# Optimization experiments

Measured on AMD Instinct MI355X. Metric: run time of the kernel, lower is better.

Reference implementation:

```python
import jax, jax.numpy as jnp
import numpy as np

B, N, D = 8, 4096, 256
H = W = 64          # grid_size = img_size // patch_size = 256 // 4
WS = 8              # swin window size
NH = 8              # swin heads
M = 16              # fno modes
E = 4               # num experts
TD = 768            # text dim
HID = 1024          # mlp hidden = 4 * D
TK = 2              # top_k


def gelu(x):
    return jax.nn.gelu(x, approximate=False)


def layernorm(x, g, b, eps=1e-5):
    mu = x.mean(-1, keepdims=True)
    var = ((x - mu) ** 2).mean(-1, keepdims=True)
    return (x - mu) * jax.lax.rsqrt(var + eps) * g + b


def fno_expert(x, w1r, w1i, w2r, w2i, conv_w, conv_b):
    # x: [B, N, D] -> grid [B, D, H, W]
    xg = x.transpose(0, 2, 1).reshape(B, D, H, W)
    xft = jnp.fft.rfft2(xg)                      # [B, D, H, W//2+1] complex64
    w1 = w1r + 1j * w1i
    w2 = w2r + 1j * w2i
    top = jnp.einsum('bixy,ioxy->boxy', xft[:, :, :M, :M], w1)
    bot = jnp.einsum('bixy,ioxy->boxy', xft[:, :, -M:, :M], w2)
    out_ft = jnp.zeros((B, D, H, W // 2 + 1), dtype=xft.dtype)
    out_ft = out_ft.at[:, :, :M, :M].set(top).at[:, :, -M:, :M].set(bot)
    x1 = jnp.fft.irfft2(out_ft, s=(H, W))        # [B, D, H, W]
    x2 = jnp.einsum('bdhw,do->bohw', xg, conv_w) + conv_b[None, :, None, None]
    out = gelu(x1 + x2)
    return out.reshape(B, D, N).transpose(0, 2, 1) + x


def mlp_expert(x, w1, b1, w2, b2):
    return gelu(x @ w1 + b1) @ w2 + b2 + x


def window_attn_expert(x, ln1_g, ln1_b, qkv_w, qkv_b, out_w, out_b,
                       ln2_g, ln2_b, mw1, mb1, mw2, mb2):
    shortcut = x
    h = layernorm(x, ln1_g, ln1_b)
    # window partition: [B,H,W,C] -> [B*nW, WS*WS, C]
    h = h.reshape(B, H // WS, WS, W // WS, WS, D)
    h = h.transpose(0, 1, 3, 2, 4, 5).reshape(-1, WS * WS, D)
    # multi-head self attention (torch nn.MultiheadAttention semantics)
    qkv = h @ qkv_w + qkv_b                      # [Bw, L, 3D]
    q, k, v = jnp.split(qkv, 3, axis=-1)
    dh = D // NH
    def heads(t):
        return t.reshape(-1, WS * WS, NH, dh).transpose(0, 2, 1, 3)
    q, k, v = heads(q), heads(k), heads(v)
    scores = jnp.einsum('whld,whmd->whlm', q, k) / jnp.sqrt(jnp.float32(dh))
    attn = jax.nn.softmax(scores, axis=-1)
    o = jnp.einsum('whlm,whmd->whld', attn, v)
    o = o.transpose(0, 2, 1, 3).reshape(-1, WS * WS, D)
    o = o @ out_w + out_b
    # window reverse
    o = o.reshape(B, H // WS, W // WS, WS, WS, D)
    o = o.transpose(0, 1, 3, 2, 4, 5).reshape(B, N, D)
    x = o + shortcut
    h2 = layernorm(x, ln2_g, ln2_b)
    return x + (gelu(h2 @ mw1 + mb1) @ mw2 + mb2)


def setup_inputs() -> dict:
    key = jax.random.key(0)
    ks = jax.random.split(key, 24)
    rn = lambda k, s: jax.random.normal(k, s, jnp.float32) * 0.02
    fscale = 1.0 / (D * D)
    ru = lambda k: jax.random.uniform(k, (D, D, M, M), jnp.float32) * fscale
    return {
        'x': jax.random.normal(ks[0], (B, N, D), jnp.float32),
        'text_embedding': jax.random.normal(ks[1], (B, TD), jnp.float32),
        'gate_w1': rn(ks[2], (D + TD, D)), 'gate_b1': jnp.zeros((D,), jnp.float32),
        'gate_w2': rn(ks[3], (D, E)), 'gate_b2': jnp.zeros((E,), jnp.float32),
        'fno_w1r': ru(ks[4]), 'fno_w1i': ru(ks[5]),
        'fno_w2r': ru(ks[6]), 'fno_w2i': ru(ks[7]),
        'fno_conv_w': rn(ks[8], (D, D)), 'fno_conv_b': jnp.zeros((D,), jnp.float32),
        'mlp1_w1': rn(ks[9], (D, HID)), 'mlp1_b1': jnp.zeros((HID,), jnp.float32),
        'mlp1_w2': rn(ks[10], (HID, D)), 'mlp1_b2': jnp.zeros((D,), jnp.float32),
        'mlp2_w1': rn(ks[11], (D, HID)), 'mlp2_b1': jnp.zeros((HID,), jnp.float32),
        'mlp2_w2': rn(ks[12], (HID, D)), 'mlp2_b2': jnp.zeros((D,), jnp.float32),
        'wa_ln1_g': jnp.ones((D,), jnp.float32), 'wa_ln1_b': jnp.zeros((D,), jnp.float32),
        'wa_qkv_w': rn(ks[13], (D, 3 * D)), 'wa_qkv_b': jnp.zeros((3 * D,), jnp.float32),
        'wa_out_w': rn(ks[14], (D, D)), 'wa_out_b': jnp.zeros((D,), jnp.float32),
        'wa_ln2_g': jnp.ones((D,), jnp.float32), 'wa_ln2_b': jnp.zeros((D,), jnp.float32),
        'wa_mlp_w1': rn(ks[15], (D, HID)), 'wa_mlp_b1': jnp.zeros((HID,), jnp.float32),
        'wa_mlp_w2': rn(ks[16], (HID, D)), 'wa_mlp_b2': jnp.zeros((D,), jnp.float32),
    }


def reference(x, text_embedding, gate_w1, gate_b1, gate_w2, gate_b2,
              fno_w1r, fno_w1i, fno_w2r, fno_w2i, fno_conv_w, fno_conv_b,
              mlp1_w1, mlp1_b1, mlp1_w2, mlp1_b2,
              mlp2_w1, mlp2_b1, mlp2_w2, mlp2_b2,
              wa_ln1_g, wa_ln1_b, wa_qkv_w, wa_qkv_b, wa_out_w, wa_out_b,
              wa_ln2_g, wa_ln2_b, wa_mlp_w1, wa_mlp_b1, wa_mlp_w2, wa_mlp_b2):
    # --- gating ---
    feat = jnp.concatenate([x.mean(axis=1), text_embedding], axis=1)  # [B, D+TD]
    logits = jax.nn.relu(feat @ gate_w1 + gate_b1) @ gate_w2 + gate_b2  # [B, E]
    top_v, top_i = jax.lax.top_k(logits, TK)
    weights = jax.nn.softmax(top_v, axis=-1)                           # [B, TK]
    # per-expert combined weight: cw[b,e] = sum_k w[b,k] * (idx[b,k]==e)
    cw = (jax.nn.one_hot(top_i, E, dtype=x.dtype) * weights[..., None]).sum(axis=1)  # [B, E]
    # --- experts (FNO, MLP, WindowAttn, MLP) ---
    e0 = fno_expert(x, fno_w1r, fno_w1i, fno_w2r, fno_w2i, fno_conv_w, fno_conv_b)
    e1 = mlp_expert(x, mlp1_w1, mlp1_b1, mlp1_w2, mlp1_b2)
    e2 = window_attn_expert(x, wa_ln1_g, wa_ln1_b, wa_qkv_w, wa_qkv_b,
                            wa_out_w, wa_out_b, wa_ln2_g, wa_ln2_b,
                            wa_mlp_w1, wa_mlp_b1, wa_mlp_w2, wa_mlp_b2)
    e3 = mlp_expert(x, mlp2_w1, mlp2_b1, mlp2_w2, mlp2_b2)
    outs = jnp.stack([e0, e1, e2, e3])                                 # [E, B, N, D]
    final = jnp.einsum('be,ebnd->bnd', cw, outs)
    return final, weights
```

## Files before the change

### kernel.cpp

```cpp
#include <hip/hip_runtime.h>
#include <math.h>


#define NB 8
#define NN 4096
#define DD 256

typedef __attribute__((ext_vector_type(8))) short bf16x8;
typedef __attribute__((ext_vector_type(4))) float f32x4;

__device__ __forceinline__ float gelu_f(float v) {
    return 0.5f * v * (1.0f + erff(v * 0.7071067811865475f));
}
__device__ __forceinline__ ushort f2bf(float f) {
    uint32_t u = __float_as_uint(f);
    uint32_t r = (u + 0x7fffu + ((u >> 16) & 1u)) >> 16;
    return (ushort)r;
}
__device__ __forceinline__ float b2f(ushort h) {
    return __uint_as_float(((uint32_t)h) << 16);
}

__global__ void k_cvt_gate(const float* __restrict__ src, ushort* __restrict__ dst,
                           float* __restrict__ gp) {
    __shared__ float4 st[4][64];
    int blk = blockIdx.x;
    int t = threadIdx.x;
    int i = blk * 256 + t;
    float4 v = ((const float4*)src)[i];
    ushort4 o;
    o.x = f2bf(v.x); o.y = f2bf(v.y); o.z = f2bf(v.z); o.w = f2bf(v.w);
    ((ushort4*)dst)[i] = o;
    st[t >> 6][t & 63] = v;
    __syncthreads();
    if (t < 64) {
        float4 a = st[0][t], b = st[1][t], c = st[2][t], d = st[3][t];
        float4 s;
        s.x = a.x + b.x + c.x + d.x;
        s.y = a.y + b.y + c.y + d.y;
        s.z = a.z + b.z + c.z + d.z;
        s.w = a.w + b.w + c.w + d.w;
        ((float4*)(gp + (size_t)blk * 256))[t] = s;
    }
}

__global__ void __launch_bounds__(256) k_gate_mm(const float* __restrict__ gp,
        const float* __restrict__ text, const float* __restrict__ w1,
        const float* __restrict__ b1, float* __restrict__ h1) {
    __shared__ float fs[1024];
    int b = blockIdx.x, t = threadIdx.x;
    const float* base = gp + (size_t)b * 1024 * 256;
    float s0 = 0.f, s1 = 0.f, s2 = 0.f, s3 = 0.f;
    for (int j = 0; j < 1024; j += 4) {
        s0 += base[(j + 0) * 256 + t];
        s1 += base[(j + 1) * 256 + t];
        s2 += base[(j + 2) * 256 + t];
        s3 += base[(j + 3) * 256 + t];
    }
    fs[t] = (s0 + s1 + s2 + s3) * (1.0f / NN);
    for (int j = t; j < 768; j += 256) fs[256 + j] = text[b * 768 + j];
    __syncthreads();
    float acc = b1[t];
    for (int k = 0; k < 1024; ++k) acc += fs[k] * w1[k * 256 + t];
    h1[b * 256 + t] = fmaxf(acc, 0.f);
}

__global__ void k_gate_top(const float* __restrict__ h1, const float* __restrict__ w2,
                           const float* __restrict__ b2, float* __restrict__ cw,
                           float* __restrict__ wout) {
    __shared__ float lg[8][4];
    int t = threadIdx.x;
    if (t < 32) {
        int b = t >> 2, e = t & 3;
        float acc = b2[e];
        const float* h = h1 + b * 256;
        for (int k = 0; k < 256; ++k) acc += h[k] * w2[k * 4 + e];
        lg[b][e] = acc;
    }
    __syncthreads();
    if (t < 8) {
        int b = t;
        float v[4];
        #pragma unroll
        for (int e = 0; e < 4; ++e) v[e] = lg[b][e];
        int i0 = 0;
        #pragma unroll
        for (int e = 1; e < 4; ++e) if (v[e] > v[i0]) i0 = e;
        int i1 = -1;
        #pragma unroll
        for (int e = 0; e < 4; ++e) {
            if (e == i0) continue;
            if (i1 < 0 || v[e] > v[i1]) i1 = e;
        }
        float v0 = v[i0], v1 = v[i1];
        float e1v = expf(v1 - v0);
        float inv = 1.0f / (1.0f + e1v);
        float w0 = inv, w1v = e1v * inv;
        wout[b * 2 + 0] = w0;
        wout[b * 2 + 1] = w1v;
        float c[4] = {0.f, 0.f, 0.f, 0.f};
        c[i0] += w0; c[i1] += w1v;
        #pragma unroll
        for (int e = 0; e < 4; ++e) cw[b * 4 + e] = c[e];
    }
}

__global__ void k_wt_all(const float* s0, const float* s1, const float* s2,
        const float* s3, const float* s4, const float* s5, const float* s6,
        const float* s7, const float* s8,
        ushort* d0, ushort* d1, ushort* d2, ushort* d3, ushort* d4,
        ushort* d5, ushort* d6, ushort* d7, ushort* d8) {
    const float* srcs[9] = {s0, s1, s2, s3, s4, s5, s6, s7, s8};
    ushort* dsts[9] = {d0, d1, d2, d3, d4, d5, d6, d7, d8};
    const int Ks[9] = {256, 1024, 256, 1024, 256, 1024, 256, 256, 256};
    const int Ns[9] = {1024, 256, 1024, 256, 1024, 256, 768, 256, 256};
    __shared__ float tile[32][33];
    int j = blockIdx.z;
    int K = Ks[j], N = Ns[j];
    int tn = N >> 5, tk = K >> 5;
    int tid = blockIdx.x;
    if (tid >= tn * tk) return;
    int n0 = (tid % tn) * 32, k0 = (tid / tn) * 32;
    const float* src = srcs[j];
    ushort* dst = dsts[j];
    int tx = threadIdx.x, ty = threadIdx.y;
    #pragma unroll
    for (int i = 0; i < 4; ++i)
        tile[ty + i * 8][tx] = src[(size_t)(k0 + ty + i * 8) * N + n0 + tx];
    __syncthreads();
    #pragma unroll
    for (int i = 0; i < 4; ++i)
        dst[(size_t)(n0 + ty + i * 8) * K + k0 + tx] = f2bf(tile[tx][ty + i * 8]);
}

template<int MODE>
__global__ void __launch_bounds__(256) k_gemm(const ushort* __restrict__ A,
        const ushort* __restrict__ Bt, const float* __restrict__ bias,
        const float* __restrict__ res, float* __restrict__ outf,
        ushort* __restrict__ outb, const float* __restrict__ cw, int eidx,
        int K, int Ncols, size_t bsA, size_t bsB, size_t bsC) {
    __shared__ alignas(16) char smem[32768];
    ushort* sA = (ushort*)smem;
    ushort* sB = (ushort*)(smem + 16384);
    int z = blockIdx.z;
    A += z * bsA; Bt += z * bsB;
    if (outf) outf += z * bsC;
    if (outb) outb += z * bsC;
    int m0 = blockIdx.x * 128;
    int n0 = blockIdx.y * 128;
    int t = threadIdx.x;
    int lane = t & 63, wid = t >> 6;
    int wr = wid >> 1, wc = wid & 1;
    int rlo = lane & 15, khi = (lane >> 4) * 8;

    auto stage = [&](int buf, int k0) {
        const ushort* Ab = A + (size_t)m0 * K + k0;
        const ushort* Bb = Bt + (size_t)n0 * K + k0;
        #pragma unroll
        for (int h = 0; h < 2; ++h) {
            int s = t + h * 256;
            int row = s >> 2, kc = (s & 3) * 8;
            __builtin_amdgcn_global_load_lds(
                (const __attribute__((address_space(1))) void*)(Ab + (size_t)row * K + kc),
                (__attribute__((address_space(3))) void*)(sA + buf * 4096 + s * 8),
                16, 0, 0);
            __builtin_amdgcn_global_load_lds(
                (const __attribute__((address_space(1))) void*)(Bb + (size_t)row * K + kc),
                (__attribute__((address_space(3))) void*)(sB + buf * 4096 + s * 8),
                16, 0, 0);
        }
    };

    f32x4 acc[4][4];
    #pragma unroll
    for (int i = 0; i < 4; ++i)
        #pragma unroll
        for (int j = 0; j < 4; ++j) acc[i][j] = (f32x4){0.f, 0.f, 0.f, 0.f};

    int KT = K >> 5;
    stage(0, 0);
    int cur = 0;
    for (int kt = 0; kt < KT; ++kt) {
        __syncthreads();
        if (kt + 1 < KT) stage(cur ^ 1, (kt + 1) << 5);
        const ushort* Ap = sA + cur * 4096;
        const ushort* Bp = sB + cur * 4096;
        bf16x8 af[4], bfr[4];
        #pragma unroll
        for (int i = 0; i < 4; ++i) {
            af[i]  = *(const bf16x8*)(Ap + (wr * 64 + i * 16 + rlo) * 32 + khi);
            bfr[i] = *(const bf16x8*)(Bp + (wc * 64 + i * 16 + rlo) * 32 + khi);
        }
        #pragma unroll
        for (int i = 0; i < 4; ++i)
            #pragma unroll
            for (int j = 0; j < 4; ++j)
                acc[i][j] = __builtin_amdgcn_mfma_f32_16x16x32_bf16(af[i], bfr[j], acc[i][j], 0, 0, 0);
        cur ^= 1;
    }

    float bj4[4];
    if constexpr (MODE != 4 && MODE != 5) {
        #pragma unroll
        for (int nt = 0; nt < 4; ++nt) bj4[nt] = bias[n0 + wc * 64 + nt * 16 + rlo];
    }

    if constexpr (MODE == 0 || MODE == 1 || MODE == 5) {
        ushort* eb = (ushort*)smem;
        #pragma unroll
        for (int mt = 0; mt < 4; ++mt) {
            __syncthreads();
            #pragma unroll
            for (int nt = 0; nt < 4; ++nt) {
                int col = wc * 64 + nt * 16 + rlo;
                #pragma unroll
                for (int j = 0; j < 4; ++j) {
                    float v = acc[mt][nt][j];
                    if constexpr (MODE == 5)
                        v += bias[m0 + wr * 64 + mt * 16 + (lane >> 4) * 4 + j];
                    else
                        v += bj4[nt];
                    if (MODE == 0) v = gelu_f(v);
                    eb[(wr * 16 + (lane >> 4) * 4 + j) * 136 + col] = f2bf(v);
                }
            }
            __syncthreads();
            #pragma unroll
            for (int h = 0; h < 2; ++h) {
                int s = t + h * 256;
                int r = s >> 4, c = (s & 15) * 8;
                int grow = m0 + (r >> 4) * 64 + mt * 16 + (r & 15);
                *(uint4*)(outb + (size_t)grow * Ncols + n0 + c) = *(uint4*)&eb[r * 136 + c];
            }
        }
    } else {
        float* ep = (float*)smem;
        #pragma unroll
        for (int mt = 0; mt < 4; ++mt) {
            __syncthreads();
            #pragma unroll
            for (int nt = 0; nt < 4; ++nt) {
                int col = wc * 64 + nt * 16 + rlo;
                #pragma unroll
                for (int j = 0; j < 4; ++j) {
                    float v = acc[mt][nt][j];
                    if constexpr (MODE == 4)
                        v += bias[m0 + wr * 64 + mt * 16 + (lane >> 4) * 4 + j];
                    else
                        v += bj4[nt];
                    ep[(wr * 16 + (lane >> 4) * 4 + j) * 132 + col] = v;
                }
            }
            __syncthreads();
            #pragma unroll
            for (int h = 0; h < 4; ++h) {
                int s = t + h * 256;
                int r = s >> 5, c4 = (s & 31) * 4;
                int grow = m0 + (r >> 4) * 64 + mt * 16 + (r & 15);
                size_t g = (size_t)grow * Ncols + n0 + c4;
                float4 v = *(float4*)&ep[r * 132 + c4];
                if constexpr (MODE == 2) {
                    if (res) {
                        float4 rv = *(const float4*)&res[g];
                        v.x += rv.x; v.y += rv.y; v.z += rv.z; v.w += rv.w;
                    }
                    *(float4*)&outf[g] = v;
                } else if constexpr (MODE == 4) {
                    *(float4*)&outf[g] = v;
                } else {
                    float cwv = cw[(grow >> 12) * 4 + eidx];
                    float4 rv = *(const float4*)&res[g];
                    float4 ov = *(float4*)&outf[g];
                    ov.x += cwv * (v.x + rv.x);
                    ov.y += cwv * (v.y + rv.y);
                    ov.z += cwv * (v.z + rv.z);
                    ov.w += cwv * (v.w + rv.w);
                    *(float4*)&outf[g] = ov;
                }
            }
        }
    }
}

__global__ void k_transpose(const ushort* __restrict__ x, ushort* __restrict__ xg) {
    __shared__ ushort tile[32][34];
    int b = blockIdx.z;
    int nt = blockIdx.x, dt = blockIdx.y;
    int tx = threadIdx.x, ty = threadIdx.y;
    const ushort* xb = x + (size_t)b * NN * DD;
    ushort* xgb = xg + (size_t)b * DD * NN;
    #pragma unroll
    for (int i = 0; i < 4; ++i) {
        int n = nt * 32 + ty + i * 8;
        tile[ty + i * 8][tx] = xb[(size_t)n * DD + dt * 32 + tx];
    }
    __syncthreads();
    #pragma unroll
    for (int i = 0; i < 4; ++i) {
        int d = dt * 32 + ty + i * 8;
        xgb[(size_t)d * NN + nt * 32 + tx] = tile[tx][ty + i * 8];
    }
}

__global__ void __launch_bounds__(256) k_rfft2(const ushort* __restrict__ xg, float* __restrict__ xft) {
    __shared__ float plane[64][65];
    __shared__ float s1re[16][66], s1im[16][66];
    __shared__ float twc[64], tws[64];
    int p = blockIdx.x;
    int t = threadIdx.x;
    int tx = t & 63, grp = t >> 6;
    const ushort* src = xg + (size_t)p * 4096;
    #pragma unroll
    for (int i = 0; i < 16; ++i) {
        int row = grp * 16 + i;
        plane[row][tx] = b2f(src[row * 64 + tx]);
    }
    if (t < 64) {
        twc[t] = cosf((float)t * (6.283185307179586f / 64.0f));
        tws[t] = sinf((float)t * (6.283185307179586f / 64.0f));
    }
    __syncthreads();
    int r = tx;
    #pragma unroll
    for (int q = 0; q < 4; ++q) {
        int kw = grp + q * 4;
        float re = 0.f, im = 0.f;
        for (int w = 0; w < 64; ++w) {
            int j = (w * kw) & 63;
            float xv = plane[r][w];
            re += xv * twc[j];
            im -= xv * tws[j];
        }
        s1re[kw][r] = re;
        s1im[kw][r] = im;
    }
    __syncthreads();
    float2* dst = (float2*)xft + (size_t)p * 512;
    #pragma unroll
    for (int q = 0; q < 2; ++q) {
        int oi = t + q * 256;
        int krow = oi >> 4, kw = oi & 15;
        int kh = krow < 16 ? krow : krow + 32;
        float re = 0.f, im = 0.f;
        for (int h = 0; h < 64; ++h) {
            int j = (h * kh) & 63;
            float c = twc[j], s = tws[j];
            float ar = s1re[kw][h], ai = s1im[kw][h];
            re += ar * c + ai * s;
            im += ai * c - ar * s;
        }
        dst[oi] = make_float2(re, im);
    }
}

__global__ void __launch_bounds__(512) k_spectral(const float* __restrict__ xft,
        const float* __restrict__ w1r, const float* __restrict__ w1i,
        const float* __restrict__ w2r, const float* __restrict__ w2i,
        float* __restrict__ part) {
    __shared__ alignas(16) ushort Wl[16 * 640];
    __shared__ alignas(16) ushort Xl[16 * 640];
    int z = blockIdx.z;
    int region = z >> 1, is = z & 1;
    const float* wrp = region ? w2r : w1r;
    const float* wip = region ? w2i : w1i;
    int xm = blockIdx.y;
    int krow = region * 16 + xm;
    int o0 = blockIdx.x * 16;
    int t = threadIdx.x;
    int wv = t >> 6, lane = t & 63;
    int rlo = lane & 15, khi = lane >> 4;
    int ibase = is * 128;

    int wy4 = t & 3, wol = (t >> 2) & 15, wi8 = t >> 6;

    f32x4 acc[2][2];
    #pragma unroll
    for (int a = 0; a < 2; ++a)
        #pragma unroll
        for (int b = 0; b < 2; ++b) acc[a][b] = (f32x4){0.f, 0.f, 0.f, 0.f};

    for (int ch = 0; ch < 4; ++ch) {
        int i0 = ibase + ch * 32;
        int ig = i0 + wi8 * 4;
        __syncthreads();
        {
            float4 f[4];
            #pragma unroll
            for (int u = 0; u < 4; ++u)
                f[u] = *(const float4*)&wrp[((size_t)(ig + u) * 256 + o0 + wol) * 256 + xm * 16 + wy4 * 4];
            #pragma unroll
            for (int yy2 = 0; yy2 < 4; ++yy2) {
                int y = wy4 * 4 + yy2;
                ushort4 pk;
                pk.x = f2bf(((const float*)&f[0])[yy2]);
                pk.y = f2bf(((const float*)&f[1])[yy2]);
                pk.z = f2bf(((const float*)&f[2])[yy2]);
                pk.w = f2bf(((const float*)&f[3])[yy2]);
                *(ushort4*)&Wl[y * 640 + wol * 40 + wi8 * 4] = pk;
            }
        }
        {
            #pragma unroll
            for (int s = 0; s < 2; ++s) {
                int m = t + s * 512;
                int y = m & 15, i4 = (m >> 4) & 7, b = (m >> 7) & 7;
                int igx = i0 + i4 * 4;
                float2 g[4];
                #pragma unroll
                for (int u = 0; u < 4; ++u)
                    g[u] = *(const float2*)&xft[(((size_t)(b * 256 + igx + u)) * 32 + krow) * 32 + y * 2];
                ushort4 re, im;
                re.x = f2bf(g[0].x); re.y = f2bf(g[1].x); re.z = f2bf(g[2].x); re.w = f2bf(g[3].x);
                im.x = f2bf(g[0].y); im.y = f2bf(g[1].y); im.z = f2bf(g[2].y); im.w = f2bf(g[3].y);
                *(ushort4*)&Xl[b * 640 + y * 40 + i4 * 4] = re;
                *(ushort4*)&Xl[(b + 8) * 640 + y * 40 + i4 * 4] = im;
            }
        }
        __syncthreads();
        #pragma unroll
        for (int yy = 0; yy < 2; ++yy) {
            int y = wv * 2 + yy;
            bf16x8 Bf = *(const bf16x8*)&Xl[rlo * 640 + y * 40 + khi * 8];
            bf16x8 Af = *(const bf16x8*)&Wl[y * 640 + rlo * 40 + khi * 8];
            acc[yy][0] = __builtin_amdgcn_mfma_f32_16x16x32_bf16(Af, Bf, acc[yy][0], 0, 0, 0);
        }
        __syncthreads();
        {
            float4 f[4];
            #pragma unroll
            for (int u = 0; u < 4; ++u)
                f[u] = *(const float4*)&wip[((size_t)(ig + u) * 256 + o0 + wol) * 256 + xm * 16 + wy4 * 4];
            #pragma unroll
            for (int yy2 = 0; yy2 < 4; ++yy2) {
                int y = wy4 * 4 + yy2;
                ushort4 pk;
                pk.x = f2bf(((const float*)&f[0])[yy2]);
                pk.y = f2bf(((const float*)&f[1])[yy2]);
                pk.z = f2bf(((const float*)&f[2])[yy2]);
                pk.w = f2bf(((const float*)&f[3])[yy2]);
                *(ushort4*)&Wl[y * 640 + wol * 40 + wi8 * 4] = pk;
            }
        }
        __syncthreads();
        #pragma unroll
        for (int yy = 0; yy < 2; ++yy) {
            int y = wv * 2 + yy;
            bf16x8 Bf = *(const bf16x8*)&Xl[rlo * 640 + y * 40 + khi * 8];
            bf16x8 Af = *(const bf16x8*)&Wl[y * 640 + rlo * 40 + khi * 8];
            acc[yy][1] = __builtin_amdgcn_mfma_f32_16x16x32_bf16(Af, Bf, acc[yy][1], 0, 0, 0);
        }
    }

    float* dp = part + (size_t)is * 4194304;
    int b = rlo & 7, hi = rlo >> 3;
    #pragma unroll
    for (int yy = 0; yy < 2; ++yy) {
        int y = wv * 2 + yy;
        #pragma unroll
        for (int j = 0; j < 4; ++j) {
            float C1 = acc[yy][0][j];
            float c2x = __shfl_xor(acc[yy][1][j], 8);
            float val = hi ? (c2x + C1) : (C1 - c2x);
            int o = o0 + khi * 4 + j;
            dp[(((size_t)(b * 256 + o) * 32 + krow) * 16 + y) * 2 + hi] = val;
        }
    }
}

__global__ void __launch_bounds__(256) k_irfft_fuse(const float* __restrict__ part,
        const ushort* __restrict__ x2t, ushort* __restrict__ tmp) {
    __shared__ float F[32][16][2];
    __shared__ float tre[16][66], tim[16][66];
    __shared__ float twc[64], tws[64];
    int p = blockIdx.x;
    int t = threadIdx.x;
    const float2* s0 = (const float2*)part + (size_t)p * 512;
    #pragma unroll
    for (int l = 0; l < 2; ++l) {
        int idx = t + l * 256;
        float2 a = s0[idx];
        float2 b2 = s0[idx + 2097152];
        ((float2*)F)[idx] = make_float2(a.x + b2.x, a.y + b2.y);
    }
    if (t < 64) {
        twc[t] = cosf((float)t * (6.283185307179586f / 64.0f));
        tws[t] = sinf((float)t * (6.283185307179586f / 64.0f));
    }
    __syncthreads();
    int h = t & 63;
    #pragma unroll
    for (int q = 0; q < 4; ++q) {
        int kw = (t >> 6) + q * 4;
        float re = 0.f, im = 0.f;
        #pragma unroll
        for (int krow = 0; krow < 32; ++krow) {
            int kh = krow < 16 ? krow : krow + 32;
            int j = (h * kh) & 63;
            float c = twc[j], s = tws[j];
            float fr = F[krow][kw][0], fi = F[krow][kw][1];
            re += fr * c - fi * s;
            im += fr * s + fi * c;
        }
        tre[kw][h] = re * (1.f / 64.f);
        tim[kw][h] = im * (1.f / 64.f);
    }
    __syncthreads();
    const ushort* x2p = x2t + (size_t)p * 4096;
    ushort* tp = tmp + (size_t)p * 4096;
    int w = t & 63;
    #pragma unroll
    for (int qq = 0; qq < 16; ++qq) {
        int qrow = (t >> 6) + qq * 4;
        float acc = tre[0][qrow];
        #pragma unroll
        for (int kw = 1; kw < 16; ++kw) {
            int j = (w * kw) & 63;
            acc += 2.f * (tre[kw][qrow] * twc[j] - tim[kw][qrow] * tws[j]);
        }
        float x1 = acc * (1.f / 64.f);
        int idx = qrow * 64 + w;
        tp[idx] = f2bf(gelu_f(x1 + b2f(x2p[idx])));
    }
}

__global__ void k_fno_final(const ushort* __restrict__ tmp, const ushort* __restrict__ xbf,
        const float* __restrict__ cw, float* __restrict__ out) {
    __shared__ float tile[32][33];
    int b = blockIdx.z;
    int n0 = blockIdx.x * 32, d0 = blockIdx.y * 32;
    int tx = threadIdx.x, ty = threadIdx.y;
    const ushort* tb = tmp + (size_t)b * DD * NN;
    #pragma unroll
    for (int i = 0; i < 4; ++i)
        tile[ty + i * 8][tx] = b2f(tb[(size_t)(d0 + ty + i * 8) * NN + n0 + tx]);
    __syncthreads();
    float cw0 = cw[b * 4];
    #pragma unroll
    for (int i = 0; i < 4; ++i) {
        int n = n0 + ty + i * 8, d = d0 + tx;
        size_t g = ((size_t)b * NN + n) * DD + d;
        out[g] = cw0 * (tile[tx][ty + i * 8] + b2f(xbf[g]));
    }
}

__global__ void __launch_bounds__(256) k_ln(const float* __restrict__ in, const float* __restrict__ g,
        const float* __restrict__ be, ushort* __restrict__ outb) {
    int row = blockIdx.x * 4 + (threadIdx.x >> 6);
    int lane = threadIdx.x & 63;
    const float4* rp = (const float4*)(in + (size_t)row * 256);
    float4 v = rp[lane];
    float s = v.x + v.y + v.z + v.w;
    float s2 = v.x * v.x + v.y * v.y + v.z * v.z + v.w * v.w;
    #pragma unroll
    for (int off = 32; off > 0; off >>= 1) {
        s += __shfl_down(s, off);
        s2 += __shfl_down(s2, off);
    }
    s = __shfl(s, 0); s2 = __shfl(s2, 0);
    float mu = s * (1.f / 256.f);
    float var = s2 * (1.f / 256.f) - mu * mu;
    float rstd = rsqrtf(var + 1e-5f);
    float4 gv = ((const float4*)g)[lane];
    float4 bv = ((const float4*)be)[lane];
    ushort4 ov;
    ov.x = f2bf((v.x - mu) * rstd * gv.x + bv.x);
    ov.y = f2bf((v.y - mu) * rstd * gv.y + bv.y);
    ov.z = f2bf((v.z - mu) * rstd * gv.z + bv.z);
    ov.w = f2bf((v.w - mu) * rstd * gv.w + bv.w);
    ((ushort4*)(outb + (size_t)row * 256))[lane] = ov;
}

__global__ void __launch_bounds__(256) k_window_attn(const ushort* __restrict__ qkvb,
        ushort* __restrict__ aob) {
    __shared__ ushort lds[4 * 7424];
    int t = threadIdx.x;
    int w = t >> 6, lane = t & 63;
    int wi = blockIdx.x, hh = blockIdx.y;
    int hd = hh * 4 + w;
    int b = wi >> 6, hb = (wi >> 3) & 7, wb = wi & 7;
    ushort* A = lds + w * 7424;
    ushort* Kl = A + 2560;
    ushort* Vt = A + 5120;
    int rlo = lane & 15, kq = lane >> 4;

    int tok = lane;
    int n = hb * 512 + wb * 8 + ((tok >> 3) << 6) + (tok & 7);
    const ushort* gq = qkvb + ((size_t)b * 4096 + n) * 768 + hd * 32;
    const uint4* qp = (const uint4*)gq;
    const uint4* kp = (const uint4*)(gq + 256);
    const uint4* vp = (const uint4*)(gq + 512);
    uint4 q0 = qp[0], q1 = qp[1], q2 = qp[2], q3 = qp[3];
    uint4 k0 = kp[0], k1 = kp[1], k2 = kp[2], k3 = kp[3];
    uint4 v0 = vp[0], v1 = vp[1], v2 = vp[2], v3 = vp[3];
    uint4* qr = (uint4*)(A + tok * 40);
    qr[0] = q0; qr[1] = q1; qr[2] = q2; qr[3] = q3;
    uint4* kr = (uint4*)(Kl + tok * 40);
    kr[0] = k0; kr[1] = k1; kr[2] = k2; kr[3] = k3;
    ushort vbuf[32];
    *(uint4*)&vbuf[0] = v0; *(uint4*)&vbuf[8] = v1;
    *(uint4*)&vbuf[16] = v2; *(uint4*)&vbuf[24] = v3;
    #pragma unroll
    for (int d = 0; d < 32; ++d) Vt[d * 72 + tok] = vbuf[d];
    __syncthreads();

    bf16x8 Qf[4], Kf[4];
    #pragma unroll
    for (int lt = 0; lt < 4; ++lt)
        Qf[lt] = *(const bf16x8*)(A + (lt * 16 + rlo) * 40 + kq * 8);
    #pragma unroll
    for (int mt = 0; mt < 4; ++mt)
        Kf[mt] = *(const bf16x8*)(Kl + (mt * 16 + rlo) * 40 + kq * 8);

    f32x4 S[4][4];
    #pragma unroll
    for (int lt = 0; lt < 4; ++lt)
        #pragma unroll
        for (int mt = 0; mt < 4; ++mt)
            S[lt][mt] = __builtin_amdgcn_mfma_f32_16x16x32_bf16(Qf[lt], Kf[mt],
                        (f32x4){0.f, 0.f, 0.f, 0.f}, 0, 0, 0);
    __syncthreads();

    const float scale = 0.17677669529663687f;
    float inv_[4][4];
    #pragma unroll
    for (int lt = 0; lt < 4; ++lt) {
        float m4[4], s4[4];
        #pragma unroll
        for (int j = 0; j < 4; ++j) {
            m4[j] = fmaxf(fmaxf(S[lt][0][j], S[lt][1][j]), fmaxf(S[lt][2][j], S[lt][3][j]));
        }
        #pragma unroll
        for (int off = 1; off < 16; off <<= 1)
            #pragma unroll
            for (int j = 0; j < 4; ++j) m4[j] = fmaxf(m4[j], __shfl_xor(m4[j], off));
        #pragma unroll
        for (int j = 0; j < 4; ++j) s4[j] = 0.f;
        #pragma unroll
        for (int mt = 0; mt < 4; ++mt)
            #pragma unroll
            for (int j = 0; j < 4; ++j) {
                float p = expf((S[lt][mt][j] - m4[j]) * scale);
                s4[j] += p;
                A[(lt * 16 + kq * 4 + j) * 72 + mt * 16 + rlo] = f2bf(p);
            }
        #pragma unroll
        for (int off = 1; off < 16; off <<= 1)
            #pragma unroll
            for (int j = 0; j < 4; ++j) s4[j] += __shfl_xor(s4[j], off);
        #pragma unroll
        for (int j = 0; j < 4; ++j) inv_[lt][j] = 1.0f / s4[j];
    }
    __syncthreads();

    f32x4 O[4][2];
    #pragma unroll
    for (int lt = 0; lt < 4; ++lt)
        #pragma unroll
        for (int dt = 0; dt < 2; ++dt) {
            f32x4 o = (f32x4){0.f, 0.f, 0.f, 0.f};
            #pragma unroll
            for (int mc = 0; mc < 2; ++mc) {
                bf16x8 pa = *(const bf16x8*)(A + (lt * 16 + rlo) * 72 + mc * 32 + kq * 8);
                bf16x8 vb = *(const bf16x8*)(Vt + (dt * 16 + rlo) * 72 + mc * 32 + kq * 8);
                o = __builtin_amdgcn_mfma_f32_16x16x32_bf16(pa, vb, o, 0, 0, 0);
            }
            O[lt][dt] = o;
        }
    __syncthreads();

    #pragma unroll
    for (int lt = 0; lt < 4; ++lt)
        #pragma unroll
        for (int dt = 0; dt < 2; ++dt)
            #pragma unroll
            for (int j = 0; j < 4; ++j)
                A[(lt * 16 + kq * 4 + j) * 40 + dt * 16 + rlo] = f2bf(O[lt][dt][j] * inv_[lt][j]);
    __syncthreads();
    const uint4* orow = (const uint4*)(A + lane * 40);
    uint4 o0 = orow[0], o1 = orow[1], o2 = orow[2], o3 = orow[3];
    uint4* gout = (uint4*)(aob + ((size_t)b * 4096 + n) * 256 + hd * 32);
    gout[0] = o0; gout[1] = o1; gout[2] = o2; gout[3] = o3;
}

extern "C" void kernel_launch(void* const* d_in, const int* in_sizes, int n_in,
                              void* d_out, int out_size, void* d_ws, size_t ws_size,
                              hipStream_t stream) {
    (void)in_sizes; (void)n_in; (void)out_size; (void)ws_size;
    const float* x        = (const float*)d_in[0];
    const float* text     = (const float*)d_in[1];
    const float* gate_w1  = (const float*)d_in[2];
    const float* gate_b1  = (const float*)d_in[3];
    const float* gate_w2  = (const float*)d_in[4];
    const float* gate_b2  = (const float*)d_in[5];
    const float* fno_w1r  = (const float*)d_in[6];
    const float* fno_w1i  = (const float*)d_in[7];
    const float* fno_w2r  = (const float*)d_in[8];
    const float* fno_w2i  = (const float*)d_in[9];
    const float* fno_cw   = (const float*)d_in[10];
    const float* fno_cb   = (const float*)d_in[11];
    const float* mlp1_w1  = (const float*)d_in[12];
    const float* mlp1_b1  = (const float*)d_in[13];
    const float* mlp1_w2  = (const float*)d_in[14];
    const float* mlp1_b2  = (const float*)d_in[15];
    const float* mlp2_w1  = (const float*)d_in[16];
    const float* mlp2_b1  = (const float*)d_in[17];
    const float* mlp2_w2  = (const float*)d_in[18];
    const float* mlp2_b2  = (const float*)d_in[19];
    const float* ln1_g    = (const float*)d_in[20];
    const float* ln1_b    = (const float*)d_in[21];
    const float* qkv_w    = (const float*)d_in[22];
    const float* qkv_b    = (const float*)d_in[23];
    const float* out_w    = (const float*)d_in[24];
    const float* out_b    = (const float*)d_in[25];
    const float* ln2_g    = (const float*)d_in[26];
    const float* ln2_b    = (const float*)d_in[27];
    const float* wa_w1    = (const float*)d_in[28];
    const float* wa_b1    = (const float*)d_in[29];
    const float* wa_w2    = (const float*)d_in[30];
    const float* wa_b2    = (const float*)d_in[31];

    float* ws   = (float*)d_ws;
    float* h1   = ws + 8192;
    float* cwp  = ws + 10240;
    ushort* wbf = (ushort*)(ws + 16384);
    ushort* w1aT = wbf;
    ushort* w2aT = w1aT + 262144;
    ushort* w1bT = w2aT + 262144;
    ushort* w2bT = w1bT + 262144;
    ushort* w1cT = w2bT + 262144;
    ushort* w2cT = w1cT + 262144;
    ushort* qkvT = w2cT + 262144;
    ushort* outwT = qkvT + 196608;
    ushort* convT = outwT + 65536;
    ushort* Xbf  = (ushort*)(ws + 16384 + 1048576);
    float* slotA = ws + 16384 + 1048576 + 4194304;
    ushort* abf  = (ushort*)slotA;
    float* xft   = slotA + 8388608;
    float* oft   = xft + 2097152;
    float* regD  = oft + 2097152;
    ushort* bigb = (ushort*)(regD + 8388608);
    float* gpart = oft;

    float* outp = (float*)d_out;
    float* wout = outp + (size_t)NB * NN * DD;

    k_cvt_gate<<<8192, 256, 0, stream>>>(x, Xbf, gpart);
    k_gate_mm<<<8, 256, 0, stream>>>(gpart, text, gate_w1, gate_b1, h1);
    k_gate_top<<<1, 64, 0, stream>>>(h1, gate_w2, gate_b2, cwp, wout);

    k_wt_all<<<dim3(256, 1, 9), dim3(32, 8), 0, stream>>>(
        mlp1_w1, mlp1_w2, mlp2_w1, mlp2_w2, wa_w1, wa_w2, qkv_w, out_w, fno_cw,
        w1aT, w2aT, w1bT, w2bT, w1cT, w2cT, qkvT, outwT, convT);

    k_transpose<<<dim3(128, 8, 8), dim3(32, 8), 0, stream>>>(Xbf, (ushort*)slotA);
    k_rfft2<<<2048, 256, 0, stream>>>((const ushort*)slotA, xft);
    k_gemm<5><<<dim3(2, 32, 8), 256, 0, stream>>>(convT, Xbf, fno_cb, nullptr, nullptr,
        (ushort*)regD, nullptr, 0, 256, 4096, 0, (size_t)NN * DD, (size_t)DD * NN);
    k_spectral<<<dim3(16, 16, 4), 512, 0, stream>>>(xft, fno_w1r, fno_w1i, fno_w2r, fno_w2i, slotA);
    k_irfft_fuse<<<2048, 256, 0, stream>>>(slotA, (const ushort*)regD, bigb);
    k_fno_final<<<dim3(128, 8, 8), dim3(32, 8), 0, stream>>>(bigb, Xbf, cwp, outp);

    k_gemm<0><<<dim3(256, 8), 256, 0, stream>>>(Xbf, w1aT, mlp1_b1, nullptr, nullptr, bigb, nullptr, 0, 256, 1024, 0, 0, 0);
    k_gemm<3><<<dim3(256, 2), 256, 0, stream>>>(bigb, w2aT, mlp1_b2, x, outp, nullptr, cwp, 1, 1024, 256, 0, 0, 0);

    k_ln<<<8192, 256, 0, stream>>>(x, ln1_g, ln1_b, abf);
    k_gemm<1><<<dim3(256, 6), 256, 0, stream>>>(abf, qkvT, qkv_b, nullptr, nullptr, bigb, nullptr, 0, 256, 768, 0, 0, 0);
    k_window_attn<<<dim3(512, 2), 256, 0, stream>>>(bigb, abf);
    k_gemm<2><<<dim3(256, 2), 256, 0, stream>>>(abf, outwT, out_b, x, regD, nullptr, nullptr, 0, 256, 256, 0, 0, 0);
    k_ln<<<8192, 256, 0, stream>>>(regD, ln2_g, ln2_b, abf);
    k_gemm<0><<<dim3(256, 8), 256, 0, stream>>>(abf, w1cT, wa_b1, nullptr, nullptr, bigb, nullptr, 0, 256, 1024, 0, 0, 0);
    k_gemm<3><<<dim3(256, 2), 256, 0, stream>>>(bigb, w2cT, wa_b2, regD, outp, nullptr, cwp, 2, 1024, 256, 0, 0, 0);

    k_gemm<0><<<dim3(256, 8), 256, 0, stream>>>(Xbf, w1bT, mlp2_b1, nullptr, nullptr, bigb, nullptr, 0, 256, 1024, 0, 0, 0);
    k_gemm<3><<<dim3(256, 2), 256, 0, stream>>>(bigb, w2bT, mlp2_b2, x, outp, nullptr, cwp, 3, 1024, 256, 0, 0, 0);
}
```

Before: 683.1 us.

## Store expert outputs in bf16 and combine them in a single final kernel

Expert GEMM epilogues now write bf16 outputs to separate buffers instead of doing fp32 read-modify-write accumulation into the output. A new k_combine kernel applies the gate weights and residuals in one pass. The window-attention residual path and the layernorm inputs switch from fp32 to bf16, and the fp32 epilogue paths are removed. This reduces fp32 traffic and the repeated read-modify-write of the output, but adds bf16 rounding on the intermediates and residuals, which may affect accuracy.

```diff
diff --git a/kernel.cpp b/kernel.cpp
--- a/kernel.cpp
+++ b/kernel.cpp
@@ -136,7 +136,7 @@
 template<int MODE>
 __global__ void __launch_bounds__(256) k_gemm(const ushort* __restrict__ A,
         const ushort* __restrict__ Bt, const float* __restrict__ bias,
-        const float* __restrict__ res, float* __restrict__ outf,
+        const void* __restrict__ res, float* __restrict__ outf,
         ushort* __restrict__ outb, const float* __restrict__ cw, int eidx,
         int K, int Ncols, size_t bsA, size_t bsB, size_t bsC) {
     __shared__ alignas(16) char smem[32768];
@@ -200,83 +200,45 @@
     }
 
     float bj4[4];
-    if constexpr (MODE != 4 && MODE != 5) {
+    if constexpr (MODE != 5) {
         #pragma unroll
         for (int nt = 0; nt < 4; ++nt) bj4[nt] = bias[n0 + wc * 64 + nt * 16 + rlo];
     }
 
-    if constexpr (MODE == 0 || MODE == 1 || MODE == 5) {
-        ushort* eb = (ushort*)smem;
-        #pragma unroll
-        for (int mt = 0; mt < 4; ++mt) {
-            __syncthreads();
-            #pragma unroll
-            for (int nt = 0; nt < 4; ++nt) {
-                int col = wc * 64 + nt * 16 + rlo;
+    ushort* eb = (ushort*)smem;
+    const ushort* resb = (const ushort*)res;
+    #pragma unroll
+    for (int mt = 0; mt < 4; ++mt) {
+        __syncthreads();
+        #pragma unroll
+        for (int nt = 0; nt < 4; ++nt) {
+            int col = wc * 64 + nt * 16 + rlo;
+            #pragma unroll
+            for (int j = 0; j < 4; ++j) {
+                float v = acc[mt][nt][j];
+                if constexpr (MODE == 5)
+                    v += bias[m0 + wr * 64 + mt * 16 + (lane >> 4) * 4 + j];
+                else
+                    v += bj4[nt];
+                if (MODE == 0) v = gelu_f(v);
+                eb[(wr * 16 + (lane >> 4) * 4 + j) * 136 + col] = f2bf(v);
+            }
+        }
+        __syncthreads();
+        #pragma unroll
+        for (int h = 0; h < 2; ++h) {
+            int s = t + h * 256;
+            int r = s >> 4, c = (s & 15) * 8;
+            int grow = m0 + (r >> 4) * 64 + mt * 16 + (r & 15);
+            if constexpr (MODE == 6) {
+                ushort ee[8], rr[8], oo[8];
+                *(uint4*)ee = *(uint4*)&eb[r * 136 + c];
+                *(uint4*)rr = *(const uint4*)(resb + (size_t)grow * Ncols + n0 + c);
                 #pragma unroll
-                for (int j = 0; j < 4; ++j) {
-                    float v = acc[mt][nt][j];
-                    if constexpr (MODE == 5)
-                        v += bias[m0 + wr * 64 + mt * 16 + (lane >> 4) * 4 + j];
-                    else
-                        v += bj4[nt];
-                    if (MODE == 0) v = gelu_f(v);
-                    eb[(wr * 16 + (lane >> 4) * 4 + j) * 136 + col] = f2bf(v);
-                }
-            }
-            __syncthreads();
-            #pragma unroll
-            for (int h = 0; h < 2; ++h) {
-                int s = t + h * 256;
-                int r = s >> 4, c = (s & 15) * 8;
-                int grow = m0 + (r >> 4) * 64 + mt * 16 + (r & 15);
+                for (int q = 0; q < 8; ++q) oo[q] = f2bf(b2f(ee[q]) + b2f(rr[q]));
+                *(uint4*)(outb + (size_t)grow * Ncols + n0 + c) = *(uint4*)oo;
+            } else {
                 *(uint4*)(outb + (size_t)grow * Ncols + n0 + c) = *(uint4*)&eb[r * 136 + c];
-            }
-        }
-    } else {
-        float* ep = (float*)smem;
-        #pragma unroll
-        for (int mt = 0; mt < 4; ++mt) {
-            __syncthreads();
-            #pragma unroll
-            for (int nt = 0; nt < 4; ++nt) {
-                int col = wc * 64 + nt * 16 + rlo;
-                #pragma unroll
-                for (int j = 0; j < 4; ++j) {
-                    float v = acc[mt][nt][j];
-                    if constexpr (MODE == 4)
-                        v += bias[m0 + wr * 64 + mt * 16 + (lane >> 4) * 4 + j];
-                    else
-                        v += bj4[nt];
-                    ep[(wr * 16 + (lane >> 4) * 4 + j) * 132 + col] = v;
-                }
-            }
-            __syncthreads();
-            #pragma unroll
-            for (int h = 0; h < 4; ++h) {
-                int s = t + h * 256;
-                int r = s >> 5, c4 = (s & 31) * 4;
-                int grow = m0 + (r >> 4) * 64 + mt * 16 + (r & 15);
-                size_t g = (size_t)grow * Ncols + n0 + c4;
-                float4 v = *(float4*)&ep[r * 132 + c4];
-                if constexpr (MODE == 2) {
-                    if (res) {
-                        float4 rv = *(const float4*)&res[g];
-                        v.x += rv.x; v.y += rv.y; v.z += rv.z; v.w += rv.w;
-                    }
-                    *(float4*)&outf[g] = v;
-                } else if constexpr (MODE == 4) {
-                    *(float4*)&outf[g] = v;
-                } else {
-                    float cwv = cw[(grow >> 12) * 4 + eidx];
-                    float4 rv = *(const float4*)&res[g];
-                    float4 ov = *(float4*)&outf[g];
-                    ov.x += cwv * (v.x + rv.x);
-                    ov.y += cwv * (v.y + rv.y);
-                    ov.z += cwv * (v.z + rv.z);
-                    ov.w += cwv * (v.w + rv.w);
-                    *(float4*)&outf[g] = ov;
-                }
             }
         }
     }
@@ -523,32 +485,53 @@
     }
 }
 
-__global__ void k_fno_final(const ushort* __restrict__ tmp, const ushort* __restrict__ xbf,
-        const float* __restrict__ cw, float* __restrict__ out) {
-    __shared__ float tile[32][33];
+__global__ void k_fno_final(const ushort* __restrict__ tmp, ushort* __restrict__ e0t) {
+    __shared__ ushort tile[32][34];
     int b = blockIdx.z;
     int n0 = blockIdx.x * 32, d0 = blockIdx.y * 32;
     int tx = threadIdx.x, ty = threadIdx.y;
     const ushort* tb = tmp + (size_t)b * DD * NN;
     #pragma unroll
     for (int i = 0; i < 4; ++i)
-        tile[ty + i * 8][tx] = b2f(tb[(size_t)(d0 + ty + i * 8) * NN + n0 + tx]);
-    __syncthreads();
-    float cw0 = cw[b * 4];
+        tile[ty + i * 8][tx] = tb[(size_t)(d0 + ty + i * 8) * NN + n0 + tx];
+    __syncthreads();
     #pragma unroll
     for (int i = 0; i < 4; ++i) {
         int n = n0 + ty + i * 8, d = d0 + tx;
-        size_t g = ((size_t)b * NN + n) * DD + d;
-        out[g] = cw0 * (tile[tx][ty + i * 8] + b2f(xbf[g]));
-    }
-}
-
-__global__ void __launch_bounds__(256) k_ln(const float* __restrict__ in, const float* __restrict__ g,
+        e0t[((size_t)b * NN + n) * DD + d] = tile[tx][ty + i * 8];
+    }
+}
+
+__global__ void __launch_bounds__(256) k_combine(const ushort* __restrict__ e0t,
+        const ushort* __restrict__ g1, const ushort* __restrict__ g2,
+        const ushort* __restrict__ g3, const ushort* __restrict__ xbf,
+        const ushort* __restrict__ xat, const float* __restrict__ cw,
+        float* __restrict__ out) {
+    int i = blockIdx.x * 256 + threadIdx.x;
+    int b = i >> 18;
+    float c0 = cw[b * 4 + 0], c1 = cw[b * 4 + 1];
+    float c2 = cw[b * 4 + 2], c3 = cw[b * 4 + 3];
+    float cx = c0 + c1 + c3;
+    ushort4 a0 = ((const ushort4*)e0t)[i];
+    ushort4 a1 = ((const ushort4*)g1)[i];
+    ushort4 a2 = ((const ushort4*)g2)[i];
+    ushort4 a3 = ((const ushort4*)g3)[i];
+    ushort4 xb = ((const ushort4*)xbf)[i];
+    ushort4 xa = ((const ushort4*)xat)[i];
+    float4 o;
+    o.x = c0 * b2f(a0.x) + c1 * b2f(a1.x) + c2 * (b2f(a2.x) + b2f(xa.x)) + c3 * b2f(a3.x) + cx * b2f(xb.x);
+    o.y = c0 * b2f(a0.y) + c1 * b2f(a1.y) + c2 * (b2f(a2.y) + b2f(xa.y)) + c3 * b2f(a3.y) + cx * b2f(xb.y);
+    o.z = c0 * b2f(a0.z) + c1 * b2f(a1.z) + c2 * (b2f(a2.z) + b2f(xa.z)) + c3 * b2f(a3.z) + cx * b2f(xb.z);
+    o.w = c0 * b2f(a0.w) + c1 * b2f(a1.w) + c2 * (b2f(a2.w) + b2f(xa.w)) + c3 * b2f(a3.w) + cx * b2f(xb.w);
+    ((float4*)out)[i] = o;
+}
+
+__global__ void __launch_bounds__(256) k_ln(const ushort* __restrict__ in, const float* __restrict__ g,
         const float* __restrict__ be, ushort* __restrict__ outb) {
     int row = blockIdx.x * 4 + (threadIdx.x >> 6);
     int lane = threadIdx.x & 63;
-    const float4* rp = (const float4*)(in + (size_t)row * 256);
-    float4 v = rp[lane];
+    ushort4 u = ((const ushort4*)(in + (size_t)row * 256))[lane];
+    float4 v = make_float4(b2f(u.x), b2f(u.y), b2f(u.z), b2f(u.w));
     float s = v.x + v.y + v.z + v.w;
     float s2 = v.x * v.x + v.y * v.y + v.z * v.z + v.w * v.w;
     #pragma unroll
@@ -734,13 +717,21 @@
     ushort* convT = outwT + 65536;
     ushort* Xbf  = (ushort*)(ws + 16384 + 1048576);
     float* slotA = ws + 16384 + 1048576 + 4194304;
-    ushort* abf  = (ushort*)slotA;
     float* xft   = slotA + 8388608;
     float* oft   = xft + 2097152;
     float* regD  = oft + 2097152;
     ushort* bigb = (ushort*)(regD + 8388608);
     float* gpart = oft;
 
+    ushort* xgb   = (ushort*)slotA;
+    ushort* g1b   = (ushort*)slotA;
+    ushort* g2b   = (ushort*)(slotA + 4194304);
+    ushort* x2tb  = (ushort*)regD;
+    ushort* e0tb  = (ushort*)regD;
+    ushort* scr   = (ushort*)(regD + 4194304);
+    ushort* g3b   = (ushort*)(regD + 4194304);
+    ushort* xatb  = (ushort*)xft;
+
     float* outp = (float*)d_out;
     float* wout = outp + (size_t)NB * NN * DD;
 
@@ -752,25 +743,27 @@
         mlp1_w1, mlp1_w2, mlp2_w1, mlp2_w2, wa_w1, wa_w2, qkv_w, out_w, fno_cw,
         w1aT, w2aT, w1bT, w2bT, w1cT, w2cT, qkvT, outwT, convT);
 
-    k_transpose<<<dim3(128, 8, 8), dim3(32, 8), 0, stream>>>(Xbf, (ushort*)slotA);
-    k_rfft2<<<2048, 256, 0, stream>>>((const ushort*)slotA, xft);
+    k_transpose<<<dim3(128, 8, 8), dim3(32, 8), 0, stream>>>(Xbf, xgb);
+    k_rfft2<<<2048, 256, 0, stream>>>(xgb, xft);
     k_gemm<5><<<dim3(2, 32, 8), 256, 0, stream>>>(convT, Xbf, fno_cb, nullptr, nullptr,
-        (ushort*)regD, nullptr, 0, 256, 4096, 0, (size_t)NN * DD, (size_t)DD * NN);
+        x2tb, nullptr, 0, 256, 4096, 0, (size_t)NN * DD, (size_t)DD * NN);
     k_spectral<<<dim3(16, 16, 4), 512, 0, stream>>>(xft, fno_w1r, fno_w1i, fno_w2r, fno_w2i, slotA);
-    k_irfft_fuse<<<2048, 256, 0, stream>>>(slotA, (const ushort*)regD, bigb);
-    k_fno_final<<<dim3(128, 8, 8), dim3(32, 8), 0, stream>>>(bigb, Xbf, cwp, outp);
+    k_irfft_fuse<<<2048, 256, 0, stream>>>(slotA, x2tb, bigb);
+    k_fno_final<<<dim3(128, 8, 8), dim3(32, 8), 0, stream>>>(bigb, e0tb);
 
     k_gemm<0><<<dim3(256, 8), 256, 0, stream>>>(Xbf, w1aT, mlp1_b1, nullptr, nullptr, bigb, nullptr, 0, 256, 1024, 0, 0, 0);
-    k_gemm<3><<<dim3(256, 2), 256, 0, stream>>>(bigb, w2aT, mlp1_b2, x, outp, nullptr, cwp, 1, 1024, 256, 0, 0, 0);
-
-    k_ln<<<8192, 256, 0, stream>>>(x, ln1_g, ln1_b, abf);
-    k_gemm<1><<<dim3(256, 6), 256, 0, stream>>>(abf, qkvT, qkv_b, nullptr, nullptr, bigb, nullptr, 0, 256, 768, 0, 0, 0);
-    k_window_attn<<<dim3(512, 2), 256, 0, stream>>>(bigb, abf);
-    k_gemm<2><<<dim3(256, 2), 256, 0, stream>>>(abf, outwT, out_b, x, regD, nullptr, nullptr, 0, 256, 256, 0, 0, 0);
-    k_ln<<<8192, 256, 0, stream>>>(regD, ln2_g, ln2_b, abf);
-    k_gemm<0><<<dim3(256, 8), 256, 0, stream>>>(abf, w1cT, wa_b1, nullptr, nullptr, bigb, nullptr, 0, 256, 1024, 0, 0, 0);
-    k_gemm<3><<<dim3(256, 2), 256, 0, stream>>>(bigb, w2cT, wa_b2, regD, outp, nullptr, cwp, 2, 1024, 256, 0, 0, 0);
+    k_gemm<1><<<dim3(256, 2), 256, 0, stream>>>(bigb, w2aT, mlp1_b2, nullptr, nullptr, g1b, nullptr, 0, 1024, 256, 0, 0, 0);
+
+    k_ln<<<8192, 256, 0, stream>>>(Xbf, ln1_g, ln1_b, scr);
+    k_gemm<1><<<dim3(256, 6), 256, 0, stream>>>(scr, qkvT, qkv_b, nullptr, nullptr, bigb, nullptr, 0, 256, 768, 0, 0, 0);
+    k_window_attn<<<dim3(512, 2), 256, 0, stream>>>(bigb, scr);
+    k_gemm<6><<<dim3(256, 2), 256, 0, stream>>>(scr, outwT, out_b, Xbf, nullptr, xatb, nullptr, 0, 256, 256, 0, 0, 0);
+    k_ln<<<8192, 256, 0, stream>>>(xatb, ln2_g, ln2_b, scr);
+    k_gemm<0><<<dim3(256, 8), 256, 0, stream>>>(scr, w1cT, wa_b1, nullptr, nullptr, bigb, nullptr, 0, 256, 1024, 0, 0, 0);
+    k_gemm<1><<<dim3(256, 2), 256, 0, stream>>>(bigb, w2cT, wa_b2, nullptr, nullptr, g2b, nullptr, 0, 1024, 256, 0, 0, 0);
 
     k_gemm<0><<<dim3(256, 8), 256, 0, stream>>>(Xbf, w1bT, mlp2_b1, nullptr, nullptr, bigb, nullptr, 0, 256, 1024, 0, 0, 0);
-    k_gemm<3><<<dim3(256, 2), 256, 0, stream>>>(bigb, w2bT, mlp2_b2, x, outp, nullptr, cwp, 3, 1024, 256, 0, 0, 0);
-}
+    k_gemm<1><<<dim3(256, 2), 256, 0, stream>>>(bigb, w2bT, mlp2_b2, nullptr, nullptr, g3b, nullptr, 0, 1024, 256, 0, 0, 0);
+
+    k_combine<<<8192, 256, 0, stream>>>(e0tb, g1b, g2b, g3b, Xbf, xatb, cwp, outp);
+}
```

Result: faster. 663.8 us (-2.8%).
